# Kernel tuning notes

Hardware: AMD Instinct MI355X
Metric: run time of the kernel (lower is better)

The kernel has to match this reference:

```python
import jax, jax.numpy as jnp
import numpy as np
import math

DIM_Q = 512; DIM_K = 512; DIM_V = 512; H = 8; EPS = 1e-5

def _layernorm(x, g, b):
    mu = jnp.mean(x, axis=-1, keepdims=True)
    var = jnp.mean((x - mu) ** 2, axis=-1, keepdims=True)
    return (x - mu) * jax.lax.rsqrt(var + EPS) * g + b

def setup_inputs() -> dict:
    key = jax.random.key(0)
    ks = jax.random.split(key, 12)
    B, NQ, NK = 8, 1024, 1024
    s = 0.02
    return {
        "Q": jax.random.normal(ks[0], (B, NQ, DIM_Q), jnp.float32),
        "K": jax.random.normal(ks[1], (B, NK, DIM_K), jnp.float32),
        "attention_mask": jax.random.randint(ks[2], (B, NK), 0, 2, jnp.int32),
        "Wq": jax.random.normal(ks[3], (DIM_Q, DIM_V), jnp.float32) * s,
        "bq": jnp.zeros((DIM_V,), jnp.float32),
        "Wk": jax.random.normal(ks[4], (DIM_K, DIM_V), jnp.float32) * s,
        "bk": jnp.zeros((DIM_V,), jnp.float32),
        "Wv": jax.random.normal(ks[5], (DIM_K, DIM_V), jnp.float32) * s,
        "bv": jnp.zeros((DIM_V,), jnp.float32),
        "Wo": jax.random.normal(ks[6], (DIM_V, DIM_V), jnp.float32) * s,
        "bo": jnp.zeros((DIM_V,), jnp.float32),
        "g0": jnp.ones((DIM_V,), jnp.float32),
        "b0": jnp.zeros((DIM_V,), jnp.float32),
        "g1": jnp.ones((DIM_V,), jnp.float32),
        "b1": jnp.zeros((DIM_V,), jnp.float32),
    }

def reference(Q, K, attention_mask, Wq, bq, Wk, bk, Wv, bv, Wo, bo, g0, b0, g1, b1):
    B, NQ, _ = Q.shape
    NK = K.shape[1]
    dh = DIM_V // H
    q = (Q @ Wq + bq).reshape(B, NQ, H, dh).transpose(0, 2, 1, 3)  # (B,H,NQ,dh)
    k = (K @ Wk + bk).reshape(B, NK, H, dh).transpose(0, 2, 1, 3)
    v = (K @ Wv + bv).reshape(B, NK, H, dh).transpose(0, 2, 1, 3)
    # NOTE: original scales by sqrt(dim_V), not sqrt(head_dim)
    scores = jnp.einsum("bhqd,bhkd->bhqk", q, k) / math.sqrt(DIM_V)
    scores = jnp.where(attention_mask[:, None, None, :] == 0, -10000.0, scores)
    A = jax.nn.softmax(scores, axis=-1)
    o = q + jnp.einsum("bhqk,bhkd->bhqd", A, v)  # residual before output proj
    O = o.transpose(0, 2, 1, 3).reshape(B, NQ, DIM_V)
    O = _layernorm(O, g0, b0)
    O = O + jax.nn.relu(O @ Wo + bo)
    O = _layernorm(O, g1, b1)
    return O
```

## Files before the change

kernel.cpp:

```cpp
#include <hip/hip_runtime.h>
#include <hip/hip_bf16.h>

typedef __attribute__((ext_vector_type(8))) short short8;
typedef __attribute__((ext_vector_type(4))) short short4v;
typedef __attribute__((ext_vector_type(4))) float float4v;
typedef __attribute__((ext_vector_type(4))) unsigned uint4v;

#define SCALE2 0.06376540791556074f
#define MBIAS2 -14426.950408889634f
#define EPST 136

__device__ inline unsigned short f2b(float f) {
    return __builtin_bit_cast(unsigned short, __float2bfloat16(f));
}
__device__ inline float b2f(unsigned short s) {
    return __uint_as_float(((unsigned)s) << 16);
}
__device__ inline unsigned pk2(float lo, float hi) {
    return (unsigned)f2b(lo) | ((unsigned)f2b(hi) << 16);
}
__device__ __forceinline__ void gld16(const unsigned short* g, unsigned short* l) {
    __builtin_amdgcn_global_load_lds(
        (const __attribute__((address_space(1))) void*)g,
        (__attribute__((address_space(3))) void*)l, 16, 0, 0);
}

__global__ void cast_bf16_kernel(const float* __restrict__ Q, const float* __restrict__ K,
                                 unsigned short* __restrict__ Qb,
                                 unsigned short* __restrict__ Kb, int n) {
    int gid = blockIdx.x * blockDim.x + threadIdx.x;
    int i = gid * 8;
    const float* in;
    unsigned short* out;
    if (i < n) { in = Q + i; out = Qb + i; }
    else       { in = K + (i - n); out = Kb + (i - n); }
    float4v a = *(const float4v*)in;
    float4v b = *(const float4v*)(in + 4);
    uint4v o = {pk2(a[0], a[1]), pk2(a[2], a[3]), pk2(b[0], b[1]), pk2(b[2], b[3])};
    *(uint4v*)out = o;
}

__global__ void transpose_w_kernel(const float* __restrict__ W0, const float* __restrict__ W1,
                                   const float* __restrict__ W2, const float* __restrict__ W3,
                                   unsigned short* __restrict__ out) {
    const float* W = (blockIdx.z == 0) ? W0 : (blockIdx.z == 1) ? W1
                   : (blockIdx.z == 2) ? W2 : W3;
    unsigned short* o = out + (size_t)blockIdx.z * 512 * 512;
    __shared__ float tile[32][33];
    int k0 = blockIdx.x * 32, n0 = blockIdx.y * 32;
    int tx = threadIdx.x & 31, ty = threadIdx.x >> 5;
    for (int r = ty; r < 32; r += 8) tile[r][tx] = W[(size_t)(k0 + r) * 512 + n0 + tx];
    __syncthreads();
    for (int r = ty; r < 32; r += 8) o[(size_t)(n0 + r) * 512 + k0 + tx] = f2b(tile[tx][r]);
}

__global__ __launch_bounds__(512) void gemm_kernel(
    const unsigned short* __restrict__ Qb, const unsigned short* __restrict__ Kb,
    const unsigned short* __restrict__ hb, const unsigned short* __restrict__ WT,
    const float* __restrict__ bq, const float* __restrict__ bk,
    const float* __restrict__ bv, const float* __restrict__ bo,
    unsigned short* __restrict__ qo, unsigned short* __restrict__ ko,
    unsigned short* __restrict__ vTo, unsigned short* __restrict__ to_,
    int zbase) {
    int z = zbase + blockIdx.z;
    const unsigned short* A = (z == 0) ? Qb : (z == 3) ? hb : Kb;
    const unsigned short* BT = WT + (size_t)z * 512 * 512;
    const float* bias = (z == 0) ? bq : (z == 1) ? bk : (z == 2) ? bv : bo;

    __shared__ unsigned short SM[4][8192];

    int tid = threadIdx.x;
    int lane = tid & 63, wave = tid >> 6;
    int wr = wave >> 2, wc = wave & 3;
    int l15 = lane & 15, lg = lane >> 4, l7 = l15 & 7;
    int row0 = blockIdx.x * 128, col0 = blockIdx.y * 128;

    float4v acc[4][2];
#pragma unroll
    for (int m = 0; m < 4; m++)
#pragma unroll
        for (int n = 0; n < 2; n++) acc[m][n] = (float4v){0.f, 0.f, 0.f, 0.f};

    int sr8 = tid >> 3;
    int gch = (tid & 7) ^ (sr8 & 7);
    const unsigned short* gA0 = A + (size_t)(row0 + sr8) * 512 + gch * 8;
    const unsigned short* gB0 = BT + (size_t)(col0 + sr8) * 512 + gch * 8;

    auto STAGE = [&](int bi, int t) {
        int k0 = t * 64;
        unsigned short* lA = SM[bi * 2] + wave * 512;
        unsigned short* lB = SM[bi * 2 + 1] + wave * 512;
#pragma unroll
        for (int c = 0; c < 2; c++) {
            gld16(gA0 + (size_t)c * 32768 + k0, lA + c * 4096);
            gld16(gB0 + (size_t)c * 32768 + k0, lB + c * 4096);
        }
    };
    auto COMPUTE = [&](int bi) {
        const unsigned short* As = SM[bi * 2];
        const unsigned short* Bs = SM[bi * 2 + 1];
#pragma unroll
        for (int kk = 0; kk < 2; kk++) {
            int ck = ((kk * 4 + lg) ^ l7) * 8;
            short8 af[4], bf[2];
#pragma unroll
            for (int m = 0; m < 4; m++)
                af[m] = *(const short8*)(As + (wr * 64 + m * 16 + l15) * 64 + ck);
#pragma unroll
            for (int n = 0; n < 2; n++)
                bf[n] = *(const short8*)(Bs + (wc * 32 + n * 16 + l15) * 64 + ck);
#pragma unroll
            for (int m = 0; m < 4; m++)
#pragma unroll
                for (int n = 0; n < 2; n++)
                    acc[m][n] = __builtin_amdgcn_mfma_f32_16x16x32_bf16(af[m], bf[n], acc[m][n], 0, 0, 0);
        }
    };

    STAGE(0, 0);
    __syncthreads();
    int buf = 0;
    for (int t = 0; t < 7; t++) {
        STAGE(buf ^ 1, t + 1);
        COMPUTE(buf);
        __syncthreads();
        buf ^= 1;
    }
    COMPUTE(buf);

    if (z == 2) {
#pragma unroll
        for (int n = 0; n < 2; n++) {
            int col = col0 + wc * 32 + n * 16 + l15;
            float bias_v = bias[col];
            int h = col >> 6, d = col & 63;
#pragma unroll
            for (int m = 0; m < 4; m++) {
                int rowb = row0 + wr * 64 + m * 16 + lg * 4;
                int b = rowb >> 10, tq = rowb & 1023;
                float4v v = acc[m][n];
                short4v st;
#pragma unroll
                for (int r = 0; r < 4; r++) st[r] = (short)f2b(v[r] + bias_v);
                *(short4v*)(vTo + ((((size_t)b * 8 + h) * 64 + d) << 10) + tq) = st;
            }
        }
    } else {
        __syncthreads();
        unsigned short* ep = &SM[0][0];
#pragma unroll
        for (int n = 0; n < 2; n++) {
            int cl = wc * 32 + n * 16 + l15;
            float bias_v = bias[col0 + cl];
#pragma unroll
            for (int m = 0; m < 4; m++) {
                float4v v = acc[m][n];
#pragma unroll
                for (int r = 0; r < 4; r++) {
                    float x = v[r] + bias_v;
                    if (z == 3) x = x > 0.f ? x : 0.f;
                    ep[(wr * 64 + m * 16 + lg * 4 + r) * EPST + cl] = f2b(x);
                }
            }
        }
        __syncthreads();
        int rr = tid >> 4, cc = (tid & 15) * 8;
        unsigned short* o = (z == 0) ? qo : (z == 1) ? ko : to_;
#pragma unroll
        for (int p = 0; p < 4; p++) {
            int row_l = p * 32 + rr;
            short8 vv = *(const short8*)(ep + row_l * EPST + cc);
            size_t gidx = (size_t)(row0 + row_l) * 512 + col0 + cc;
            if (z == 3) {
                short8 hv = *(const short8*)(hb + gidx);
                short8 o8;
#pragma unroll
                for (int j = 0; j < 8; j++)
                    o8[j] = (short)f2b(b2f((unsigned short)vv[j]) + b2f((unsigned short)hv[j]));
                *(short8*)(o + gidx) = o8;
            } else {
                *(short8*)(o + gidx) = vv;
            }
        }
    }
}

__global__ __launch_bounds__(256) void attn_kernel(
    const unsigned short* __restrict__ qb, const unsigned short* __restrict__ kb,
    const unsigned short* __restrict__ vT, const int* __restrict__ mask,
    unsigned short* __restrict__ ob) {
    __shared__ unsigned short Ks[2][64 * 64];
    __shared__ unsigned short Vs[2][64 * 64];
    __shared__ float mb[2][64];

    int tid = threadIdx.x;
    int lane = tid & 63, wave = tid >> 6;
    int l15 = lane & 15, lg = lane >> 4, l7 = l15 & 7;
    int bh = blockIdx.y;
    int b = bh >> 3, h = bh & 7;
    int qrow0 = b * 1024 + blockIdx.x * 64 + wave * 16;

    short8 qf[2];
#pragma unroll
    for (int kk = 0; kk < 2; kk++)
        qf[kk] = *(const short8*)(qb + (size_t)(qrow0 + l15) * 512 + h * 64 + kk * 32 + lg * 8);

    float l_acc = 0.f;
    float4v oacc[4];
#pragma unroll
    for (int n = 0; n < 4; n++) oacc[n] = (float4v){0.f, 0.f, 0.f, 0.f};

    int srow = tid >> 2, koff = (tid & 3) * 16;
    int kc0 = koff >> 3;
    int prow = (srow & 0x23) | ((srow & 4) << 2) | ((srow & 0x18) >> 1);
    int pk = prow & 7, sk = srow & 7;

    short8 kreg[2], vreg[2];
    float mreg = 0.f;
    auto LOADR = [&](int t) {
        const unsigned short* kg = kb + (size_t)(b * 1024 + t * 64 + srow) * 512 + h * 64 + koff;
        kreg[0] = *(const short8*)kg;
        kreg[1] = *(const short8*)(kg + 8);
        const unsigned short* vg = vT + (((size_t)bh * 64 + srow) << 10) + t * 64 + koff;
        vreg[0] = *(const short8*)vg;
        vreg[1] = *(const short8*)(vg + 8);
        if (tid < 64) mreg = mask[b * 1024 + t * 64 + tid] ? 0.f : MBIAS2;
    };
    auto WLDS = [&](int bi) {
        *(short8*)(Ks[bi] + prow * 64 + ((kc0 ^ pk) << 3))       = kreg[0];
        *(short8*)(Ks[bi] + prow * 64 + (((kc0 + 1) ^ pk) << 3)) = kreg[1];
        *(short8*)(Vs[bi] + srow * 64 + ((kc0 ^ sk) << 3))       = vreg[0];
        *(short8*)(Vs[bi] + srow * 64 + (((kc0 + 1) ^ sk) << 3)) = vreg[1];
        if (tid < 64) mb[bi][tid] = mreg;
    };

    LOADR(0);
    WLDS(0);
    __syncthreads();
    int buf = 0;
    for (int t = 0; t < 16; t++) {
        if (t < 15) LOADR(t + 1);

        const unsigned short* Kc = Ks[buf];
        const unsigned short* Vc = Vs[buf];
        float p[4][4];
#pragma unroll
        for (int jf = 0; jf < 4; jf++) {
            short8 kf0 = *(const short8*)(Kc + (jf * 16 + l15) * 64 + ((lg ^ l7) << 3));
            short8 kf1 = *(const short8*)(Kc + (jf * 16 + l15) * 64 + (((4 + lg) ^ l7) << 3));
            float4v tt = (float4v){0.f, 0.f, 0.f, 0.f};
            tt = __builtin_amdgcn_mfma_f32_16x16x32_bf16(kf0, qf[0], tt, 0, 0, 0);
            tt = __builtin_amdgcn_mfma_f32_16x16x32_bf16(kf1, qf[1], tt, 0, 0, 0);
#pragma unroll
            for (int r = 0; r < 4; r++) p[jf][r] = tt[r];
        }
#pragma unroll
        for (int jf = 0; jf < 4; jf++)
#pragma unroll
            for (int r = 0; r < 4; r++) {
                float e = exp2f(fmaf(p[jf][r], SCALE2,
                                     mb[buf][32 * (jf >> 1) + 8 * lg + 4 * (jf & 1) + r]));
                p[jf][r] = e;
                l_acc += e;
            }
        short8 pb[2];
#pragma unroll
        for (int ks = 0; ks < 2; ks++) {
            uint4v w = {pk2(p[2 * ks][0], p[2 * ks][1]), pk2(p[2 * ks][2], p[2 * ks][3]),
                        pk2(p[2 * ks + 1][0], p[2 * ks + 1][1]),
                        pk2(p[2 * ks + 1][2], p[2 * ks + 1][3])};
            pb[ks] = __builtin_bit_cast(short8, w);
        }
#pragma unroll
        for (int n = 0; n < 4; n++)
#pragma unroll
            for (int ks = 0; ks < 2; ks++) {
                short8 vf = *(const short8*)(Vc + (n * 16 + l15) * 64 + (((ks * 4 + lg) ^ l7) << 3));
                oacc[n] = __builtin_amdgcn_mfma_f32_16x16x32_bf16(vf, pb[ks], oacc[n], 0, 0, 0);
            }

        if (t < 15) {
            WLDS(buf ^ 1);
            __syncthreads();
            buf ^= 1;
        }
    }

    l_acc += __shfl_xor(l_acc, 16);
    l_acc += __shfl_xor(l_acc, 32);
    float inv = 1.f / l_acc;
#pragma unroll
    for (int n = 0; n < 4; n++) {
        size_t base = (size_t)(qrow0 + l15) * 512 + h * 64 + n * 16 + lg * 4;
        short4v qr = *(const short4v*)(qb + base);
        short4v st;
#pragma unroll
        for (int r = 0; r < 4; r++)
            st[r] = (short)f2b(b2f((unsigned short)qr[r]) + oacc[n][r] * inv);
        *(short4v*)(ob + base) = st;
    }
}

__global__ void ln_kernel_bf16(const unsigned short* __restrict__ in,
                               const float* __restrict__ g, const float* __restrict__ bb,
                               unsigned short* __restrict__ out) {
    int row = blockIdx.x, lane = threadIdx.x;
    short8 v = *(const short8*)(in + (size_t)row * 512 + lane * 8);
    float x[8], s = 0.f, s2 = 0.f;
#pragma unroll
    for (int j = 0; j < 8; j++) {
        x[j] = b2f((unsigned short)v[j]);
        s += x[j];
        s2 += x[j] * x[j];
    }
#pragma unroll
    for (int off = 1; off < 64; off <<= 1) {
        s += __shfl_xor(s, off);
        s2 += __shfl_xor(s2, off);
    }
    float mu = s * (1.f / 512.f);
    float var = s2 * (1.f / 512.f) - mu * mu;
    float rs = rsqrtf(var + 1e-5f);
#pragma unroll
    for (int j = 0; j < 8; j++) {
        int c = lane * 8 + j;
        out[(size_t)row * 512 + c] = f2b((x[j] - mu) * rs * g[c] + bb[c]);
    }
}

__global__ void ln_kernel_f32(const unsigned short* __restrict__ in,
                              const float* __restrict__ g, const float* __restrict__ bb,
                              float* __restrict__ out) {
    int row = blockIdx.x, lane = threadIdx.x;
    short8 v = *(const short8*)(in + (size_t)row * 512 + lane * 8);
    float x[8], s = 0.f, s2 = 0.f;
#pragma unroll
    for (int j = 0; j < 8; j++) {
        x[j] = b2f((unsigned short)v[j]);
        s += x[j];
        s2 += x[j] * x[j];
    }
#pragma unroll
    for (int off = 1; off < 64; off <<= 1) {
        s += __shfl_xor(s, off);
        s2 += __shfl_xor(s2, off);
    }
    float mu = s * (1.f / 512.f);
    float var = s2 * (1.f / 512.f) - mu * mu;
    float rs = rsqrtf(var + 1e-5f);
#pragma unroll
    for (int j = 0; j < 8; j++) {
        int c = lane * 8 + j;
        out[(size_t)row * 512 + c] = (x[j] - mu) * rs * g[c] + bb[c];
    }
}

extern "C" void kernel_launch(void* const* d_in, const int* in_sizes, int n_in,
                              void* d_out, int out_size, void* d_ws, size_t ws_size,
                              hipStream_t stream) {
    const float* Q = (const float*)d_in[0];
    const float* K = (const float*)d_in[1];
    const int* mask = (const int*)d_in[2];
    const float* Wq = (const float*)d_in[3];
    const float* bq = (const float*)d_in[4];
    const float* Wk = (const float*)d_in[5];
    const float* bk = (const float*)d_in[6];
    const float* Wv = (const float*)d_in[7];
    const float* bv = (const float*)d_in[8];
    const float* Wo = (const float*)d_in[9];
    const float* bo = (const float*)d_in[10];
    const float* g0 = (const float*)d_in[11];
    const float* b0 = (const float*)d_in[12];
    const float* g1 = (const float*)d_in[13];
    const float* b1 = (const float*)d_in[14];
    float* out = (float*)d_out;

    const size_t N = 8192ull * 512;
    unsigned short* w16 = (unsigned short*)d_ws;
    unsigned short* Qb = w16;
    unsigned short* Kb = Qb + N;
    unsigned short* WT = Kb + N;
    unsigned short* qb = WT + 4ull * 512 * 512;
    unsigned short* kb = qb + N;
    unsigned short* vTb = kb + N;
    unsigned short* obuf = vTb + N;
    unsigned short* hbuf = obuf + N;
    unsigned short* tbuf = hbuf + N;

    cast_bf16_kernel<<<4096, 256, 0, stream>>>(Q, K, Qb, Kb, (int)N);
    transpose_w_kernel<<<dim3(16, 16, 4), 256, 0, stream>>>(Wq, Wk, Wv, Wo, WT);
    gemm_kernel<<<dim3(64, 4, 3), 512, 0, stream>>>(Qb, Kb, hbuf, WT, bq, bk, bv, bo,
                                                    qb, kb, vTb, tbuf, 0);
    attn_kernel<<<dim3(16, 64), 256, 0, stream>>>(qb, kb, vTb, mask, obuf);
    ln_kernel_bf16<<<8192, 64, 0, stream>>>(obuf, g0, b0, hbuf);
    gemm_kernel<<<dim3(64, 4, 1), 512, 0, stream>>>(Qb, Kb, hbuf, WT, bq, bk, bv, bo,
                                                    qb, kb, vTb, tbuf, 3);
    ln_kernel_f32<<<8192, 64, 0, stream>>>(tbuf, g1, b1, out);
}
```

Measured before the change: 195.4 us.

## Merge prep kernels, triple-buffer attention with 8-wave blocks, batch LN rows

Fuses the input cast and weight transpose into a single prep launch. The attention kernel now uses 512-thread blocks covering 128 query rows, a three-stage LDS ring, and computes QK^T for the next tile before the softmax and PV of the current one, so score MFMAs overlap exp work and loads are issued further ahead. Both layernorm kernels process four rows per 256-thread block instead of one row per 64-thread block. The costs are more LDS per block and higher register pressure from the extra score buffer, which may reduce occupancy.

```diff
diff --git a/kernel.cpp b/kernel.cpp
--- a/kernel.cpp
+++ b/kernel.cpp
@@ -25,33 +25,33 @@
         (__attribute__((address_space(3))) void*)l, 16, 0, 0);
 }
 
-__global__ void cast_bf16_kernel(const float* __restrict__ Q, const float* __restrict__ K,
-                                 unsigned short* __restrict__ Qb,
-                                 unsigned short* __restrict__ Kb, int n) {
-    int gid = blockIdx.x * blockDim.x + threadIdx.x;
-    int i = gid * 8;
-    const float* in;
-    unsigned short* out;
-    if (i < n) { in = Q + i; out = Qb + i; }
-    else       { in = K + (i - n); out = Kb + (i - n); }
-    float4v a = *(const float4v*)in;
-    float4v b = *(const float4v*)(in + 4);
-    uint4v o = {pk2(a[0], a[1]), pk2(a[2], a[3]), pk2(b[0], b[1]), pk2(b[2], b[3])};
-    *(uint4v*)out = o;
-}
-
-__global__ void transpose_w_kernel(const float* __restrict__ W0, const float* __restrict__ W1,
-                                   const float* __restrict__ W2, const float* __restrict__ W3,
-                                   unsigned short* __restrict__ out) {
-    const float* W = (blockIdx.z == 0) ? W0 : (blockIdx.z == 1) ? W1
-                   : (blockIdx.z == 2) ? W2 : W3;
-    unsigned short* o = out + (size_t)blockIdx.z * 512 * 512;
+__global__ void prep_kernel(const float* __restrict__ Q, const float* __restrict__ K,
+                            const float* __restrict__ W0, const float* __restrict__ W1,
+                            const float* __restrict__ W2, const float* __restrict__ W3,
+                            unsigned short* __restrict__ Qb, unsigned short* __restrict__ Kb,
+                            unsigned short* __restrict__ WT, int n) {
     __shared__ float tile[32][33];
-    int k0 = blockIdx.x * 32, n0 = blockIdx.y * 32;
-    int tx = threadIdx.x & 31, ty = threadIdx.x >> 5;
-    for (int r = ty; r < 32; r += 8) tile[r][tx] = W[(size_t)(k0 + r) * 512 + n0 + tx];
-    __syncthreads();
-    for (int r = ty; r < 32; r += 8) o[(size_t)(n0 + r) * 512 + k0 + tx] = f2b(tile[tx][r]);
+    if (blockIdx.x < 4096) {
+        int i = (blockIdx.x * 256 + threadIdx.x) * 8;
+        const float* in;
+        unsigned short* out;
+        if (i < n) { in = Q + i; out = Qb + i; }
+        else       { in = K + (i - n); out = Kb + (i - n); }
+        float4v a = *(const float4v*)in;
+        float4v b = *(const float4v*)(in + 4);
+        uint4v o = {pk2(a[0], a[1]), pk2(a[2], a[3]), pk2(b[0], b[1]), pk2(b[2], b[3])};
+        *(uint4v*)out = o;
+    } else {
+        int bid = blockIdx.x - 4096;
+        int z = bid >> 8, rem = bid & 255;
+        const float* W = (z == 0) ? W0 : (z == 1) ? W1 : (z == 2) ? W2 : W3;
+        unsigned short* o = WT + (size_t)z * 512 * 512;
+        int k0 = (rem >> 4) * 32, n0 = (rem & 15) * 32;
+        int tx = threadIdx.x & 31, ty = threadIdx.x >> 5;
+        for (int r = ty; r < 32; r += 8) tile[r][tx] = W[(size_t)(k0 + r) * 512 + n0 + tx];
+        __syncthreads();
+        for (int r = ty; r < 32; r += 8) o[(size_t)(n0 + r) * 512 + k0 + tx] = f2b(tile[tx][r]);
+    }
 }
 
 __global__ __launch_bounds__(512) void gemm_kernel(
@@ -185,20 +185,20 @@
     }
 }
 
-__global__ __launch_bounds__(256) void attn_kernel(
+__global__ __launch_bounds__(512) void attn_kernel(
     const unsigned short* __restrict__ qb, const unsigned short* __restrict__ kb,
     const unsigned short* __restrict__ vT, const int* __restrict__ mask,
     unsigned short* __restrict__ ob) {
-    __shared__ unsigned short Ks[2][64 * 64];
-    __shared__ unsigned short Vs[2][64 * 64];
-    __shared__ float mb[2][64];
+    __shared__ unsigned short Ks[3][64 * 64];
+    __shared__ unsigned short Vs[3][64 * 64];
+    __shared__ float mb[3][64];
 
     int tid = threadIdx.x;
     int lane = tid & 63, wave = tid >> 6;
     int l15 = lane & 15, lg = lane >> 4, l7 = l15 & 7;
     int bh = blockIdx.y;
     int b = bh >> 3, h = bh & 7;
-    int qrow0 = b * 1024 + blockIdx.x * 64 + wave * 16;
+    int qrow0 = b * 1024 + blockIdx.x * 128 + wave * 16;
 
     short8 qf[2];
 #pragma unroll
@@ -210,40 +210,25 @@
 #pragma unroll
     for (int n = 0; n < 4; n++) oacc[n] = (float4v){0.f, 0.f, 0.f, 0.f};
 
-    int srow = tid >> 2, koff = (tid & 3) * 16;
-    int kc0 = koff >> 3;
+    int srow = tid >> 3, kch = tid & 7;
+    int koff = kch * 8;
     int prow = (srow & 0x23) | ((srow & 4) << 2) | ((srow & 0x18) >> 1);
-    int pk = prow & 7, sk = srow & 7;
-
-    short8 kreg[2], vreg[2];
+    int pkx = (kch ^ (prow & 7)) << 3, skx = (kch ^ (srow & 7)) << 3;
+
+    short8 kreg, vreg;
     float mreg = 0.f;
     auto LOADR = [&](int t) {
-        const unsigned short* kg = kb + (size_t)(b * 1024 + t * 64 + srow) * 512 + h * 64 + koff;
-        kreg[0] = *(const short8*)kg;
-        kreg[1] = *(const short8*)(kg + 8);
-        const unsigned short* vg = vT + (((size_t)bh * 64 + srow) << 10) + t * 64 + koff;
-        vreg[0] = *(const short8*)vg;
-        vreg[1] = *(const short8*)(vg + 8);
+        kreg = *(const short8*)(kb + (size_t)(b * 1024 + t * 64 + srow) * 512 + h * 64 + koff);
+        vreg = *(const short8*)(vT + (((size_t)bh * 64 + srow) << 10) + t * 64 + koff);
         if (tid < 64) mreg = mask[b * 1024 + t * 64 + tid] ? 0.f : MBIAS2;
     };
     auto WLDS = [&](int bi) {
-        *(short8*)(Ks[bi] + prow * 64 + ((kc0 ^ pk) << 3))       = kreg[0];
-        *(short8*)(Ks[bi] + prow * 64 + (((kc0 + 1) ^ pk) << 3)) = kreg[1];
-        *(short8*)(Vs[bi] + srow * 64 + ((kc0 ^ sk) << 3))       = vreg[0];
-        *(short8*)(Vs[bi] + srow * 64 + (((kc0 + 1) ^ sk) << 3)) = vreg[1];
+        *(short8*)(Ks[bi] + prow * 64 + pkx) = kreg;
+        *(short8*)(Vs[bi] + srow * 64 + skx) = vreg;
         if (tid < 64) mb[bi][tid] = mreg;
     };
-
-    LOADR(0);
-    WLDS(0);
-    __syncthreads();
-    int buf = 0;
-    for (int t = 0; t < 16; t++) {
-        if (t < 15) LOADR(t + 1);
-
-        const unsigned short* Kc = Ks[buf];
-        const unsigned short* Vc = Vs[buf];
-        float p[4][4];
+    auto QKT = [&](int bi, float (*S)[4]) {
+        const unsigned short* Kc = Ks[bi];
 #pragma unroll
         for (int jf = 0; jf < 4; jf++) {
             short8 kf0 = *(const short8*)(Kc + (jf * 16 + l15) * 64 + ((lg ^ l7) << 3));
@@ -252,14 +237,30 @@
             tt = __builtin_amdgcn_mfma_f32_16x16x32_bf16(kf0, qf[0], tt, 0, 0, 0);
             tt = __builtin_amdgcn_mfma_f32_16x16x32_bf16(kf1, qf[1], tt, 0, 0, 0);
 #pragma unroll
-            for (int r = 0; r < 4; r++) p[jf][r] = tt[r];
-        }
+            for (int r = 0; r < 4; r++) S[jf][r] = tt[r];
+        }
+    };
+
+    LOADR(0); WLDS(0);
+    LOADR(1); WLDS(1);
+    __syncthreads();
+    float S[4][4], Sn[4][4];
+    QKT(0, S);
+    LOADR(2);
+
+#pragma unroll
+    for (int t = 0; t < 16; t++) {
+        int cur = t % 3, nxt = (t + 1) % 3, stg = (t + 2) % 3;
+
+        if (t < 15) QKT(nxt, Sn);
+
+        float p[4][4];
 #pragma unroll
         for (int jf = 0; jf < 4; jf++)
 #pragma unroll
             for (int r = 0; r < 4; r++) {
-                float e = exp2f(fmaf(p[jf][r], SCALE2,
-                                     mb[buf][32 * (jf >> 1) + 8 * lg + 4 * (jf & 1) + r]));
+                float e = exp2f(fmaf(S[jf][r], SCALE2,
+                                     mb[cur][32 * (jf >> 1) + 8 * lg + 4 * (jf & 1) + r]));
                 p[jf][r] = e;
                 l_acc += e;
             }
@@ -271,6 +272,7 @@
                         pk2(p[2 * ks + 1][2], p[2 * ks + 1][3])};
             pb[ks] = __builtin_bit_cast(short8, w);
         }
+        const unsigned short* Vc = Vs[cur];
 #pragma unroll
         for (int n = 0; n < 4; n++)
 #pragma unroll
@@ -279,11 +281,14 @@
                 oacc[n] = __builtin_amdgcn_mfma_f32_16x16x32_bf16(vf, pb[ks], oacc[n], 0, 0, 0);
             }
 
-        if (t < 15) {
-            WLDS(buf ^ 1);
-            __syncthreads();
-            buf ^= 1;
-        }
+        if (t < 14) WLDS(stg);
+        if (t < 13) LOADR(t + 3);
+        if (t < 14) __syncthreads();
+
+#pragma unroll
+        for (int jf = 0; jf < 4; jf++)
+#pragma unroll
+            for (int r = 0; r < 4; r++) S[jf][r] = Sn[jf][r];
     }
 
     l_acc += __shfl_xor(l_acc, 16);
@@ -304,7 +309,8 @@
 __global__ void ln_kernel_bf16(const unsigned short* __restrict__ in,
                                const float* __restrict__ g, const float* __restrict__ bb,
                                unsigned short* __restrict__ out) {
-    int row = blockIdx.x, lane = threadIdx.x;
+    int row = blockIdx.x * 4 + (threadIdx.x >> 6);
+    int lane = threadIdx.x & 63;
     short8 v = *(const short8*)(in + (size_t)row * 512 + lane * 8);
     float x[8], s = 0.f, s2 = 0.f;
 #pragma unroll
@@ -331,7 +337,8 @@
 __global__ void ln_kernel_f32(const unsigned short* __restrict__ in,
                               const float* __restrict__ g, const float* __restrict__ bb,
                               float* __restrict__ out) {
-    int row = blockIdx.x, lane = threadIdx.x;
+    int row = blockIdx.x * 4 + (threadIdx.x >> 6);
+    int lane = threadIdx.x & 63;
     short8 v = *(const short8*)(in + (size_t)row * 512 + lane * 8);
     float x[8], s = 0.f, s2 = 0.f;
 #pragma unroll
@@ -387,13 +394,12 @@
     unsigned short* hbuf = obuf + N;
     unsigned short* tbuf = hbuf + N;
 
-    cast_bf16_kernel<<<4096, 256, 0, stream>>>(Q, K, Qb, Kb, (int)N);
-    transpose_w_kernel<<<dim3(16, 16, 4), 256, 0, stream>>>(Wq, Wk, Wv, Wo, WT);
+    prep_kernel<<<5120, 256, 0, stream>>>(Q, K, Wq, Wk, Wv, Wo, Qb, Kb, WT, (int)N);
     gemm_kernel<<<dim3(64, 4, 3), 512, 0, stream>>>(Qb, Kb, hbuf, WT, bq, bk, bv, bo,
                                                     qb, kb, vTb, tbuf, 0);
-    attn_kernel<<<dim3(16, 64), 256, 0, stream>>>(qb, kb, vTb, mask, obuf);
-    ln_kernel_bf16<<<8192, 64, 0, stream>>>(obuf, g0, b0, hbuf);
+    attn_kernel<<<dim3(8, 64), 512, 0, stream>>>(qb, kb, vTb, mask, obuf);
+    ln_kernel_bf16<<<2048, 256, 0, stream>>>(obuf, g0, b0, hbuf);
     gemm_kernel<<<dim3(64, 4, 1), 512, 0, stream>>>(Qb, Kb, hbuf, WT, bq, bk, bv, bo,
                                                     qb, kb, vTb, tbuf, 3);
-    ln_kernel_f32<<<8192, 64, 0, stream>>>(tbuf, g1, b1, out);
-}
+    ln_kernel_f32<<<2048, 256, 0, stream>>>(tbuf, g1, b1, out);
+}
```

Measured after the change: 217.4 us. +11.3%, slower.
